# Kernel optimization log

Hardware: AMD Instinct MI355X
Metric: run time of the kernel (lower is better)

The kernel has to match this reference:

```python
import jax, jax.numpy as jnp
import numpy as np

RADIUS = 1
KS = 2 * RADIUS + 1  # kernel_size

def setup_inputs() -> dict:
    key = jax.random.key(0)
    k1, k2 = jax.random.split(key)
    shape = (1, 32, 96, 96, 96)  # [B, C, D, H, W]
    fixed = jax.random.normal(k1, shape, dtype=jnp.float32)
    moving = jax.random.normal(k2, shape, dtype=jnp.float32)
    return {"fixed": fixed, "moving": moving}

def reference(fixed, moving):
    # Local window correlation: out[b, idx, p] = sum_c fixed[b,c,p] * moving[b,c,p+off(idx)-radius]
    # with zero padding, matching the one-hot grouped conv3d in the torch module.
    B, C, D, H, W = fixed.shape
    pad = ((0, 0), (0, 0), (RADIUS, RADIUS), (RADIUS, RADIUS), (RADIUS, RADIUS))
    mp = jnp.pad(moving, pad)  # zero-padded moving
    corrs = []
    # Offsets enumerated in the same (i, j, k) row-major order as the torch module.
    for i in range(KS):
        for j in range(KS):
            for k in range(KS):
                shifted = mp[:, :, i:i + D, j:j + H, k:k + W]  # [B,C,D,H,W]
                corrs.append(jnp.sum(fixed * shifted, axis=1))  # reduce channels
    out = jnp.stack(corrs, axis=1)  # [B, kernel_volume, D, H, W]
    scale = jnp.asarray(C, fixed.dtype) ** -0.5  # normalize=True
    return out * scale
```

## Files before the change

### kernel.cpp

```cpp
#include <hip/hip_runtime.h>

#define N 96
#define NNN (N * N * N)
#define C_CH 32

#define TXD 8
#define TYD 8
#define TZD 4
#define VX 4
#define TW (TXD * VX)
#define TH TYD
#define TD TZD

#define HWS 35
#define HH 10
#define HD 6
#define PLANE (HWS * HH)
#define HTOT (PLANE * HD)
#define NTH (TXD * TYD * TZD)
#define NR ((HTOT + NTH - 1) / NTH)
#define SMSZ (NR * NTH)

__global__ __launch_bounds__(NTH, 3) void wincorr_kernel(
    const float* __restrict__ fixedp,
    const float* __restrict__ movingp,
    float* __restrict__ outp)
{
    __shared__ float sm[SMSZ];

    const int tx = threadIdx.x;
    const int ty = threadIdx.y;
    const int tz = threadIdx.z;
    const int tid = tx + TXD * ty + TXD * TYD * tz;

    const int w0 = blockIdx.x * TW;
    const int h0 = blockIdx.y * TH;
    const int d0 = blockIdx.z * TD;

    int off[NR];
    #pragma unroll
    for (int r = 0; r < NR; ++r) {
        const int a = tid + r * NTH;
        const int z   = a / PLANE;
        const int rm  = a - z * PLANE;
        const int y   = rm / HWS;
        const int x   = rm - y * HWS;
        const int sd = d0 - 1 + z;
        const int sh = h0 - 1 + y;
        const int sw = w0 - 1 + x;
        const bool ok = (a < HTOT) && (x < 34) &&
                        ((unsigned)sd < N) && ((unsigned)sh < N) && ((unsigned)sw < N);
        off[r] = ok ? ((sd * N + sh) * N + sw) : -1;
    }

    const int gw = w0 + VX * tx;
    const int fix_base = ((d0 + tz) * N + (h0 + ty)) * N + gw;
    const int lbase = tz * PLANE + ty * HWS + VX * tx;

    float acc[27][VX];
    #pragma unroll
    for (int s = 0; s < 27; ++s)
        #pragma unroll
        for (int v = 0; v < VX; ++v) acc[s][v] = 0.0f;

    float st[NR];
    #pragma unroll
    for (int r = 0; r < NR; ++r)
        st[r] = (off[r] >= 0) ? movingp[off[r]] : 0.0f;
    float4 fnext = *(const float4*)&fixedp[fix_base];

    for (int c = 0; c < C_CH; ++c) {
        __syncthreads();
        #pragma unroll
        for (int r = 0; r < NR; ++r)
            sm[tid + r * NTH] = st[r];
        __syncthreads();

        const float4 f = fnext;
        const float fv[VX] = {f.x, f.y, f.z, f.w};

        if (c + 1 < C_CH) {
            const float* mnext = movingp + (size_t)(c + 1) * NNN;
            #pragma unroll
            for (int r = 0; r < NR; ++r)
                st[r] = (off[r] >= 0) ? mnext[off[r]] : 0.0f;
            fnext = *(const float4*)&fixedp[(size_t)(c + 1) * NNN + fix_base];
        }

        #pragma unroll
        for (int i = 0; i < 3; ++i) {
            #pragma unroll
            for (int j = 0; j < 3; ++j) {
                const float* row = &sm[lbase + i * PLANE + j * HWS];
                float wv[VX + 2];
                #pragma unroll
                for (int m = 0; m < VX + 2; ++m) wv[m] = row[m];
                #pragma unroll
                for (int k = 0; k < 3; ++k)
                    #pragma unroll
                    for (int v = 0; v < VX; ++v)
                        acc[(i * 3 + j) * 3 + k][v] += fv[v] * wv[v + k];
            }
        }
    }

    const float scale = 0.17677669529663687f;
    #pragma unroll
    for (int s = 0; s < 27; ++s) {
        float4 o;
        o.x = acc[s][0] * scale;
        o.y = acc[s][1] * scale;
        o.z = acc[s][2] * scale;
        o.w = acc[s][3] * scale;
        *(float4*)&outp[(size_t)s * NNN + fix_base] = o;
    }
}

extern "C" void kernel_launch(void* const* d_in, const int* in_sizes, int n_in,
                              void* d_out, int out_size, void* d_ws, size_t ws_size,
                              hipStream_t stream) {
    const float* fixedp  = (const float*)d_in[0];
    const float* movingp = (const float*)d_in[1];
    float* outp = (float*)d_out;

    dim3 block(TXD, TYD, TZD);
    dim3 grid(N / TW, N / TH, N / TD);
    wincorr_kernel<<<grid, block, 0, stream>>>(fixedp, movingp, outp);
}
```

Measured before the change: 291.8 us.

## Halve per-thread W vector width and double-buffer shared memory tiles

Each thread now covers 2 output columns instead of 4, so the block tile narrows to 16 in W and the shared halo row shrinks to 20. The single shared buffer is replaced by two alternating buffers, which drops one of the two barriers per channel. Launch bounds rise to 4 blocks per CU because the accumulator count is halved. The cost is a larger halo-to-output ratio, so more redundant moving-tensor loads per output and smaller vector stores; the grid and the fixed-tensor loads follow the new width automatically through TW.

```diff
diff --git a/kernel.cpp b/kernel.cpp
--- a/kernel.cpp
+++ b/kernel.cpp
@@ -7,12 +7,12 @@
 #define TXD 8
 #define TYD 8
 #define TZD 4
-#define VX 4
+#define VX 2
 #define TW (TXD * VX)
 #define TH TYD
 #define TD TZD
 
-#define HWS 35
+#define HWS 20
 #define HH 10
 #define HD 6
 #define PLANE (HWS * HH)
@@ -21,12 +21,13 @@
 #define NR ((HTOT + NTH - 1) / NTH)
 #define SMSZ (NR * NTH)
 
-__global__ __launch_bounds__(NTH, 3) void wincorr_kernel(
+__global__ __launch_bounds__(NTH, 4) void wincorr_kernel(
     const float* __restrict__ fixedp,
     const float* __restrict__ movingp,
     float* __restrict__ outp)
 {
-    __shared__ float sm[SMSZ];
+    __shared__ float smA[SMSZ];
+    __shared__ float smB[SMSZ];
 
     const int tx = threadIdx.x;
     const int ty = threadIdx.y;
@@ -48,7 +49,7 @@
         const int sd = d0 - 1 + z;
         const int sh = h0 - 1 + y;
         const int sw = w0 - 1 + x;
-        const bool ok = (a < HTOT) && (x < 34) &&
+        const bool ok = (a < HTOT) && (x < TW + 2) &&
                         ((unsigned)sd < N) && ((unsigned)sh < N) && ((unsigned)sw < N);
         off[r] = ok ? ((sd * N + sh) * N + sw) : -1;
     }
@@ -67,52 +68,56 @@
     #pragma unroll
     for (int r = 0; r < NR; ++r)
         st[r] = (off[r] >= 0) ? movingp[off[r]] : 0.0f;
-    float4 fnext = *(const float4*)&fixedp[fix_base];
+    float2 fcur = *(const float2*)&fixedp[fix_base];
+    float2 fnext = fcur;
 
-    for (int c = 0; c < C_CH; ++c) {
-        __syncthreads();
+    auto step = [&](int c, float* __restrict__ smw) {
         #pragma unroll
         for (int r = 0; r < NR; ++r)
-            sm[tid + r * NTH] = st[r];
-        __syncthreads();
-
-        const float4 f = fnext;
-        const float fv[VX] = {f.x, f.y, f.z, f.w};
+            smw[tid + r * NTH] = st[r];
 
         if (c + 1 < C_CH) {
             const float* mnext = movingp + (size_t)(c + 1) * NNN;
             #pragma unroll
             for (int r = 0; r < NR; ++r)
                 st[r] = (off[r] >= 0) ? mnext[off[r]] : 0.0f;
-            fnext = *(const float4*)&fixedp[(size_t)(c + 1) * NNN + fix_base];
+            fnext = *(const float2*)&fixedp[(size_t)(c + 1) * NNN + fix_base];
         }
 
+        __syncthreads();
+
+        const float fv0 = fcur.x;
+        const float fv1 = fcur.y;
         #pragma unroll
         for (int i = 0; i < 3; ++i) {
             #pragma unroll
             for (int j = 0; j < 3; ++j) {
-                const float* row = &sm[lbase + i * PLANE + j * HWS];
+                const float* row = &smw[lbase + i * PLANE + j * HWS];
                 float wv[VX + 2];
                 #pragma unroll
                 for (int m = 0; m < VX + 2; ++m) wv[m] = row[m];
                 #pragma unroll
-                for (int k = 0; k < 3; ++k)
-                    #pragma unroll
-                    for (int v = 0; v < VX; ++v)
-                        acc[(i * 3 + j) * 3 + k][v] += fv[v] * wv[v + k];
+                for (int k = 0; k < 3; ++k) {
+                    acc[(i * 3 + j) * 3 + k][0] += fv0 * wv[k];
+                    acc[(i * 3 + j) * 3 + k][1] += fv1 * wv[k + 1];
+                }
             }
         }
+        fcur = fnext;
+    };
+
+    for (int c = 0; c < C_CH; c += 2) {
+        step(c, smA);
+        step(c + 1, smB);
     }
 
     const float scale = 0.17677669529663687f;
     #pragma unroll
     for (int s = 0; s < 27; ++s) {
-        float4 o;
+        float2 o;
         o.x = acc[s][0] * scale;
         o.y = acc[s][1] * scale;
-        o.z = acc[s][2] * scale;
-        o.w = acc[s][3] * scale;
-        *(float4*)&outp[(size_t)s * NNN + fix_base] = o;
+        *(float2*)&outp[(size_t)s * NNN + fix_base] = o;
     }
 }
 
```

Result: slower. 301.8 us (+3.4%).

## Double-buffer LDS halo across channels with one barrier per step and nontemporal stores

Applied to the files above, without the earlier changes.

The single LDS halo buffer becomes two buffers that alternate by channel, and global prefetch now runs two channels ahead. This removes one of the two __syncthreads per channel, leaving a hand-written waitcnt plus s_barrier. Output stores become nontemporal. The cost is doubled LDS, a second set of staging registers, and launch bounds lowered from 3 to 2 waves, which may reduce occupancy.

```diff
diff --git a/kernel.cpp b/kernel.cpp
--- a/kernel.cpp
+++ b/kernel.cpp
@@ -21,12 +21,15 @@
 #define NR ((HTOT + NTH - 1) / NTH)
 #define SMSZ (NR * NTH)
 
-__global__ __launch_bounds__(NTH, 3) void wincorr_kernel(
+typedef float vfloat4 __attribute__((ext_vector_type(4)));
+
+__global__ __launch_bounds__(NTH, 2) void wincorr_kernel(
     const float* __restrict__ fixedp,
     const float* __restrict__ movingp,
     float* __restrict__ outp)
 {
-    __shared__ float sm[SMSZ];
+    __shared__ float smA[SMSZ];
+    __shared__ float smB[SMSZ];
 
     const int tx = threadIdx.x;
     const int ty = threadIdx.y;
@@ -48,7 +51,7 @@
         const int sd = d0 - 1 + z;
         const int sh = h0 - 1 + y;
         const int sw = w0 - 1 + x;
-        const bool ok = (a < HTOT) && (x < 34) &&
+        const bool ok = (a < HTOT) && (x < TW + 2) &&
                         ((unsigned)sd < N) && ((unsigned)sh < N) && ((unsigned)sw < N);
         off[r] = ok ? ((sd * N + sh) * N + sw) : -1;
     }
@@ -63,35 +66,43 @@
         #pragma unroll
         for (int v = 0; v < VX; ++v) acc[s][v] = 0.0f;
 
-    float st[NR];
+    float st0[NR], st1[NR];
     #pragma unroll
     for (int r = 0; r < NR; ++r)
-        st[r] = (off[r] >= 0) ? movingp[off[r]] : 0.0f;
-    float4 fnext = *(const float4*)&fixedp[fix_base];
-
-    for (int c = 0; c < C_CH; ++c) {
-        __syncthreads();
+        st0[r] = (off[r] >= 0) ? movingp[off[r]] : 0.0f;
+    float4 f0 = *(const float4*)&fixedp[fix_base];
+    {
+        const float* m1 = movingp + (size_t)NNN;
         #pragma unroll
         for (int r = 0; r < NR; ++r)
-            sm[tid + r * NTH] = st[r];
-        __syncthreads();
+            st1[r] = (off[r] >= 0) ? m1[off[r]] : 0.0f;
+    }
+    float4 f1 = *(const float4*)&fixedp[(size_t)NNN + fix_base];
 
-        const float4 f = fnext;
+    auto step = [&](int c, float* __restrict__ smw, float (&st)[NR], float4& f) {
+        #pragma unroll
+        for (int r = 0; r < NR; ++r)
+            smw[tid + r * NTH] = st[r];
+
         const float fv[VX] = {f.x, f.y, f.z, f.w};
 
-        if (c + 1 < C_CH) {
-            const float* mnext = movingp + (size_t)(c + 1) * NNN;
+        if (c + 2 < C_CH) {
+            const float* mn = movingp + (size_t)(c + 2) * NNN;
             #pragma unroll
             for (int r = 0; r < NR; ++r)
-                st[r] = (off[r] >= 0) ? mnext[off[r]] : 0.0f;
-            fnext = *(const float4*)&fixedp[(size_t)(c + 1) * NNN + fix_base];
+                st[r] = (off[r] >= 0) ? mn[off[r]] : 0.0f;
+            f = *(const float4*)&fixedp[(size_t)(c + 2) * NNN + fix_base];
         }
+
+        asm volatile("s_waitcnt lgkmcnt(0)" ::: "memory");
+        __builtin_amdgcn_s_barrier();
+        asm volatile("" ::: "memory");
 
         #pragma unroll
         for (int i = 0; i < 3; ++i) {
             #pragma unroll
             for (int j = 0; j < 3; ++j) {
-                const float* row = &sm[lbase + i * PLANE + j * HWS];
+                const float* row = &smw[lbase + i * PLANE + j * HWS];
                 float wv[VX + 2];
                 #pragma unroll
                 for (int m = 0; m < VX + 2; ++m) wv[m] = row[m];
@@ -102,17 +113,22 @@
                         acc[(i * 3 + j) * 3 + k][v] += fv[v] * wv[v + k];
             }
         }
+    };
+
+    for (int c = 0; c < C_CH; c += 2) {
+        step(c,     smA, st0, f0);
+        step(c + 1, smB, st1, f1);
     }
 
     const float scale = 0.17677669529663687f;
     #pragma unroll
     for (int s = 0; s < 27; ++s) {
-        float4 o;
+        vfloat4 o;
         o.x = acc[s][0] * scale;
         o.y = acc[s][1] * scale;
         o.z = acc[s][2] * scale;
         o.w = acc[s][3] * scale;
-        *(float4*)&outp[(size_t)s * NNN + fix_base] = o;
+        __builtin_nontemporal_store(o, (vfloat4*)&outp[(size_t)s * NNN + fix_base]);
     }
 }
 
```

Result: faster. 281.0 us (-3.7%).

## Replace shared-memory halo staging with direct cached global loads and nontemporal stores

Applied to the files above, without the earlier changes.

Removes the LDS halo tile and both per-channel __syncthreads. Each thread now loads its 9 neighbour rows straight from global memory as float4 plus two scalar edge values, and handles boundaries with clamped addresses and multiplicative masks. Output writes become nontemporal stores and the occupancy hint drops from 3 to 2. This removes barrier stalls and LDS traffic but relies on L1/L2 to absorb roughly 9x redundant global reads, and gives up the software prefetch of the next channel.

```diff
diff --git a/kernel.cpp b/kernel.cpp
--- a/kernel.cpp
+++ b/kernel.cpp
@@ -11,51 +11,45 @@
 #define TW (TXD * VX)
 #define TH TYD
 #define TD TZD
+#define NTH (TXD * TYD * TZD)
 
-#define HWS 35
-#define HH 10
-#define HD 6
-#define PLANE (HWS * HH)
-#define HTOT (PLANE * HD)
-#define NTH (TXD * TYD * TZD)
-#define NR ((HTOT + NTH - 1) / NTH)
-#define SMSZ (NR * NTH)
+typedef float vfloat4 __attribute__((ext_vector_type(4)));
 
-__global__ __launch_bounds__(NTH, 3) void wincorr_kernel(
+__global__ __launch_bounds__(NTH, 2) void wincorr_kernel(
     const float* __restrict__ fixedp,
     const float* __restrict__ movingp,
     float* __restrict__ outp)
 {
-    __shared__ float sm[SMSZ];
-
     const int tx = threadIdx.x;
     const int ty = threadIdx.y;
     const int tz = threadIdx.z;
-    const int tid = tx + TXD * ty + TXD * TYD * tz;
 
     const int w0 = blockIdx.x * TW;
     const int h0 = blockIdx.y * TH;
     const int d0 = blockIdx.z * TD;
 
-    int off[NR];
-    #pragma unroll
-    for (int r = 0; r < NR; ++r) {
-        const int a = tid + r * NTH;
-        const int z   = a / PLANE;
-        const int rm  = a - z * PLANE;
-        const int y   = rm / HWS;
-        const int x   = rm - y * HWS;
-        const int sd = d0 - 1 + z;
-        const int sh = h0 - 1 + y;
-        const int sw = w0 - 1 + x;
-        const bool ok = (a < HTOT) && (x < 34) &&
-                        ((unsigned)sd < N) && ((unsigned)sh < N) && ((unsigned)sw < N);
-        off[r] = ok ? ((sd * N + sh) * N + sw) : -1;
-    }
-
     const int gw = w0 + VX * tx;
     const int fix_base = ((d0 + tz) * N + (h0 + ty)) * N + gw;
-    const int lbase = tz * PLANE + ty * HWS + VX * tx;
+
+    int rowoff[9];
+    float rmf[9];
+    #pragma unroll
+    for (int i = 0; i < 3; ++i) {
+        #pragma unroll
+        for (int j = 0; j < 3; ++j) {
+            const int d = d0 + tz - 1 + i;
+            const int h = h0 + ty - 1 + j;
+            const bool ok = ((unsigned)d < N) && ((unsigned)h < N);
+            const int cd = min(max(d, 0), N - 1);
+            const int ch = min(max(h, 0), N - 1);
+            rowoff[i * 3 + j] = (cd * N + ch) * N + gw;
+            rmf[i * 3 + j] = ok ? 1.0f : 0.0f;
+        }
+    }
+    const int   dL  = (gw > 0) ? -1 : 0;
+    const int   dR  = (gw + VX < N) ? VX : VX - 1;
+    const float mwL = (gw > 0) ? 1.0f : 0.0f;
+    const float mwR = (gw + VX < N) ? 1.0f : 0.0f;
 
     float acc[27][VX];
     #pragma unroll
@@ -63,56 +57,53 @@
         #pragma unroll
         for (int v = 0; v < VX; ++v) acc[s][v] = 0.0f;
 
-    float st[NR];
-    #pragma unroll
-    for (int r = 0; r < NR; ++r)
-        st[r] = (off[r] >= 0) ? movingp[off[r]] : 0.0f;
-    float4 fnext = *(const float4*)&fixedp[fix_base];
+    for (int c = 0; c < C_CH; ++c) {
+        const float* __restrict__ p = movingp + (size_t)c * NNN;
 
-    for (int c = 0; c < C_CH; ++c) {
-        __syncthreads();
+        float4 A[9];
+        float  Cv[9];
+        float  Dv[9];
         #pragma unroll
-        for (int r = 0; r < NR; ++r)
-            sm[tid + r * NTH] = st[r];
-        __syncthreads();
-
-        const float4 f = fnext;
-        const float fv[VX] = {f.x, f.y, f.z, f.w};
-
-        if (c + 1 < C_CH) {
-            const float* mnext = movingp + (size_t)(c + 1) * NNN;
-            #pragma unroll
-            for (int r = 0; r < NR; ++r)
-                st[r] = (off[r] >= 0) ? mnext[off[r]] : 0.0f;
-            fnext = *(const float4*)&fixedp[(size_t)(c + 1) * NNN + fix_base];
+        for (int r = 0; r < 9; ++r) {
+            A[r]  = *(const float4*)(p + rowoff[r]);
+            Cv[r] = p[rowoff[r] + dL];
+            Dv[r] = p[rowoff[r] + dR];
         }
+        const float4 f = *(const float4*)&fixedp[(size_t)c * NNN + fix_base];
 
         #pragma unroll
-        for (int i = 0; i < 3; ++i) {
-            #pragma unroll
-            for (int j = 0; j < 3; ++j) {
-                const float* row = &sm[lbase + i * PLANE + j * HWS];
-                float wv[VX + 2];
-                #pragma unroll
-                for (int m = 0; m < VX + 2; ++m) wv[m] = row[m];
-                #pragma unroll
-                for (int k = 0; k < 3; ++k)
-                    #pragma unroll
-                    for (int v = 0; v < VX; ++v)
-                        acc[(i * 3 + j) * 3 + k][v] += fv[v] * wv[v + k];
-            }
+        for (int r = 0; r < 9; ++r) {
+            const float t0 = f.x * rmf[r];
+            const float t1 = f.y * rmf[r];
+            const float t2 = f.z * rmf[r];
+            const float t3 = f.w * rmf[r];
+            const float tL = t0 * mwL;
+            const float tR = t3 * mwR;
+            const int b = r * 3;
+            acc[b + 0][0] += tL * Cv[r];
+            acc[b + 0][1] += t1 * A[r].x;
+            acc[b + 0][2] += t2 * A[r].y;
+            acc[b + 0][3] += t3 * A[r].z;
+            acc[b + 1][0] += t0 * A[r].x;
+            acc[b + 1][1] += t1 * A[r].y;
+            acc[b + 1][2] += t2 * A[r].z;
+            acc[b + 1][3] += t3 * A[r].w;
+            acc[b + 2][0] += t0 * A[r].y;
+            acc[b + 2][1] += t1 * A[r].z;
+            acc[b + 2][2] += t2 * A[r].w;
+            acc[b + 2][3] += tR * Dv[r];
         }
     }
 
     const float scale = 0.17677669529663687f;
     #pragma unroll
     for (int s = 0; s < 27; ++s) {
-        float4 o;
+        vfloat4 o;
         o.x = acc[s][0] * scale;
         o.y = acc[s][1] * scale;
         o.z = acc[s][2] * scale;
         o.w = acc[s][3] * scale;
-        *(float4*)&outp[(size_t)s * NNN + fix_base] = o;
+        __builtin_nontemporal_store(o, (vfloat4*)&outp[(size_t)s * NNN + fix_base]);
     }
 }
 
```

Result: slower. 640.2 us (+119.4%).
